# Optimization experiments

Measured on AMD Instinct MI355X. Metric: run time of the kernel, lower is better.

## Reference

```python
import jax, jax.numpy as jnp
import numpy as np

EPS = 1e-12
B, S, H, NH, L, F = 8, 512, 768, 12, 12, 3072
V, TV, P = 21128, 2, 512
DH = H // NH


def layer_norm(x, g, b):
    m = jnp.mean(x, axis=-1, keepdims=True)
    v = jnp.var(x, axis=-1, keepdims=True)
    return g * (x - m) / jnp.sqrt(v + EPS) + b


def setup_inputs() -> dict:
    key = jax.random.key(0)
    ks = iter(jax.random.split(key, 40))
    r = lambda shape: (jax.random.normal(next(ks), shape, jnp.float32) * 0.02)
    inp = {
        "input_ids": jax.random.randint(next(ks), (B, S), 0, V, jnp.int32),
        "segment_ids": jax.random.randint(next(ks), (B, S), 0, TV, jnp.int32),
        "attention_mask": jnp.ones((B, 1, 1, S), jnp.float32),
        "tok_emb": r((V, H)),
        "pos_emb": r((P, H)),
        "type_emb": r((TV, H)),
        "emb_g": jnp.ones((H,), jnp.float32),
        "emb_b": jnp.zeros((H,), jnp.float32),
        # stacked per-layer params [L, ...]
        "Wq": r((L, H, H)), "bq": jnp.zeros((L, H), jnp.float32),
        "Wk": r((L, H, H)), "bk": jnp.zeros((L, H), jnp.float32),
        "Wv": r((L, H, H)), "bv": jnp.zeros((L, H), jnp.float32),
        "Wao": r((L, H, H)), "bao": jnp.zeros((L, H), jnp.float32),
        "ln1_g": jnp.ones((L, H), jnp.float32), "ln1_b": jnp.zeros((L, H), jnp.float32),
        "Wi": r((L, H, F)), "bi": jnp.zeros((L, F), jnp.float32),
        "Wio": r((L, F, H)), "bio": jnp.zeros((L, H), jnp.float32),
        "ln2_g": jnp.ones((L, H), jnp.float32), "ln2_b": jnp.zeros((L, H), jnp.float32),
    }
    return inp


def reference(input_ids, segment_ids, attention_mask,
              tok_emb, pos_emb, type_emb, emb_g, emb_b,
              Wq, bq, Wk, bk, Wv, bv, Wao, bao, ln1_g, ln1_b,
              Wi, bi, Wio, bio, ln2_g, ln2_b):
    # ---- embedding: token + type + position, then LayerNorm ----
    x = tok_emb[input_ids] + type_emb[segment_ids] + pos_emb[None, :S, :]
    x = layer_norm(x, emb_g, emb_b)  # [B,S,H]

    mask_add = (1.0 - attention_mask) * -10000.0  # [B,1,1,S]
    scale = 1.0 / jnp.sqrt(jnp.asarray(DH, x.dtype))

    def split_heads(t):  # [B,S,H] -> [B,NH,S,DH]
        return t.reshape(B, S, NH, DH).transpose(0, 2, 1, 3)

    for l in range(Wq.shape[0]):
        q = split_heads(x @ Wq[l] + bq[l])
        k = split_heads(x @ Wk[l] + bk[l])
        v = split_heads(x @ Wv[l] + bv[l])
        score = jnp.einsum("bhqd,bhkd->bhqk", q, k) * scale + mask_add
        attn = jax.nn.softmax(score, axis=-1)
        ctx = jnp.einsum("bhqk,bhkd->bhqd", attn, v)
        ctx = ctx.transpose(0, 2, 1, 3).reshape(B, S, H)
        # attention output: dense + residual + LN
        attn_out = layer_norm(ctx @ Wao[l] + bao[l] + x, ln1_g[l], ln1_b[l])
        # FFN: dense-gelu-dense + residual + LN (exact erf gelu as in tf.keras)
        h = jax.nn.gelu(attn_out @ Wi[l] + bi[l], approximate=False)
        x = layer_norm(h @ Wio[l] + bio[l] + attn_out, ln2_g[l], ln2_b[l])

    return x  # sequence output [B,S,H]
```

## Files before the change

### kernel.cpp

```cpp
#include <hip/hip_runtime.h>
#include <math.h>

static constexpr int Bc = 8;
static constexpr int Sc = 512;
static constexpr int Hc = 768;
static constexpr int NHc = 12;
static constexpr int Lc = 12;
static constexpr int Fc = 3072;
static constexpr int DHc = 64;
static constexpr int NTOK = Bc * Sc;
static constexpr int QKVN = 3 * Hc;

static constexpr size_t W_QKV_OFF = 0;
static constexpr size_t W_AO_OFF  = 1769472;
static constexpr size_t W_I_OFF   = 2359296;
static constexpr size_t W_IO_OFF  = 4718592;
static constexpr size_t LW        = 7077888;

typedef _Float16 h16x8 __attribute__((ext_vector_type(8)));
typedef float f32x4 __attribute__((ext_vector_type(4)));
typedef unsigned short us4 __attribute__((ext_vector_type(4)));
typedef unsigned short us8 __attribute__((ext_vector_type(8)));
typedef unsigned int u32x4 __attribute__((ext_vector_type(4)));

__device__ __forceinline__ unsigned short f2h(float f) {
    _Float16 h = (_Float16)f;
    return __builtin_bit_cast(unsigned short, h);
}
__device__ __forceinline__ float h2f(unsigned short u) {
    return (float)__builtin_bit_cast(_Float16, u);
}

#define AS1 __attribute__((address_space(1)))
#define AS3 __attribute__((address_space(3)))
__device__ __forceinline__ void gld_lds16(const void* g, void* l) {
    __builtin_amdgcn_global_load_lds((const AS1 void*)g, (AS3 void*)l, 16, 0, 0);
}

__global__ __launch_bounds__(256) void prep_kernel(
    const float* __restrict__ Wq, const float* __restrict__ Wk,
    const float* __restrict__ Wv, const float* __restrict__ Wao,
    const float* __restrict__ Wi, const float* __restrict__ Wio,
    const float* __restrict__ bq, const float* __restrict__ bk,
    const float* __restrict__ bv, unsigned short* __restrict__ WALL,
    float* __restrict__ BALL)
{
    int t = blockIdx.x, l = blockIdx.y;
    int tid = threadIdx.x;

    if (t >= 432) {
        int idx = (t - 432) * 256 + tid;
        float v = (idx < 768) ? bq[l * Hc + idx]
                : (idx < 1536) ? bk[l * Hc + idx - 768]
                               : bv[l * Hc + idx - 1536];
        BALL[(size_t)l * QKVN + idx] = v;
        return;
    }

    const float* src;
    unsigned short* dst;
    int K, N, nkt, local;
    if (t < 144) {
        int mat = t / 36; local = t % 36;
        K = 768; N = 768; nkt = 3;
        src = (mat == 0 ? Wq : mat == 1 ? Wk : mat == 2 ? Wv : Wao) + (size_t)l * 589824;
        dst = WALL + (size_t)l * LW + (mat < 3 ? (size_t)mat * 589824 : W_AO_OFF);
    } else if (t < 288) {
        local = t - 144; K = 768; N = 3072; nkt = 3;
        src = Wi + (size_t)l * 2359296;
        dst = WALL + (size_t)l * LW + W_I_OFF;
    } else {
        local = t - 288; K = 3072; N = 768; nkt = 12;
        src = Wio + (size_t)l * 2359296;
        dst = WALL + (size_t)l * LW + W_IO_OFF;
    }
    int n0 = (local / nkt) * 64, k0 = (local % nkt) * 256;

    __shared__ float tl[64][65];
    int tx = tid & 15, ty = tid >> 4;
    int s_own = (tid >> 3) & 3;
    int c8    = tid & 7;
    int rb    = tid >> 5;

    us8 o[8];
    for (int s = 0; s < 4; s++) {
        int ks = k0 + s * 64;
#pragma unroll
        for (int j = 0; j < 4; j++) {
            int k = ty + j * 16;
            float4 v = *(const float4*)(src + (size_t)(ks + k) * N + n0 + tx * 4);
            tl[k][tx * 4 + 0] = v.x; tl[k][tx * 4 + 1] = v.y;
            tl[k][tx * 4 + 2] = v.z; tl[k][tx * 4 + 3] = v.w;
        }
        __syncthreads();
        if (s == s_own) {
#pragma unroll
            for (int it = 0; it < 8; it++) {
                int r = rb + it * 8;
#pragma unroll
                for (int j = 0; j < 8; j++) o[it][j] = f2h(tl[c8 * 8 + j][r]);
            }
        }
        __syncthreads();
    }
#pragma unroll
    for (int it = 0; it < 8; it++) {
        int r = rb + it * 8;
        *(us8*)(dst + (size_t)(n0 + r) * K + k0 + s_own * 64 + c8 * 8) = o[it];
    }
}

__device__ __forceinline__ void ln_stats192(float4 v, float& mean, float& rstd) {
    float s = v.x + v.y + v.z + v.w;
    float s2 = v.x * v.x + v.y * v.y + v.z * v.z + v.w * v.w;
#pragma unroll
    for (int o = 32; o > 0; o >>= 1) { s += __shfl_xor(s, o); s2 += __shfl_xor(s2, o); }
    __shared__ float red[6];
    int lane = threadIdx.x & 63, wid = threadIdx.x >> 6;
    if (lane == 0) { red[wid] = s; red[3 + wid] = s2; }
    __syncthreads();
    float ts  = red[0] + red[1] + red[2];
    float ts2 = red[3] + red[4] + red[5];
    mean = ts * (1.0f / Hc);
    float var = ts2 * (1.0f / Hc) - mean * mean;
    rstd = rsqrtf(var + 1e-12f);
}

__global__ __launch_bounds__(192) void embed_ln_kernel(
    const int* __restrict__ ids, const int* __restrict__ seg,
    const float* __restrict__ tok, const float* __restrict__ typ,
    const float* __restrict__ pos, const float* __restrict__ g,
    const float* __restrict__ b, float* __restrict__ outf,
    unsigned short* __restrict__ outb)
{
    int t = blockIdx.x;
    int si = t % Sc;
    int id = ids[t], sg = seg[t];
    int i = threadIdx.x;

    float4 tv = *(const float4*)(tok + (size_t)id * Hc + 4 * i);
    float4 yv = *(const float4*)(typ + (size_t)sg * Hc + 4 * i);
    float4 pv = *(const float4*)(pos + (size_t)si * Hc + 4 * i);
    float4 v = make_float4(tv.x + yv.x + pv.x, tv.y + yv.y + pv.y,
                           tv.z + yv.z + pv.z, tv.w + yv.w + pv.w);
    float mean, rstd;
    ln_stats192(v, mean, rstd);

    float4 gv = *(const float4*)(g + 4 * i);
    float4 bv = *(const float4*)(b + 4 * i);
    float4 o = make_float4(gv.x * (v.x - mean) * rstd + bv.x,
                           gv.y * (v.y - mean) * rstd + bv.y,
                           gv.z * (v.z - mean) * rstd + bv.z,
                           gv.w * (v.w - mean) * rstd + bv.w);
    *(float4*)(outf + (size_t)t * Hc + 4 * i) = o;
    us4 ob; ob[0] = f2h(o.x); ob[1] = f2h(o.y); ob[2] = f2h(o.z); ob[3] = f2h(o.w);
    *(us4*)(outb + (size_t)t * Hc + 4 * i) = ob;
}

__global__ __launch_bounds__(192) void add_ln2h_kernel(
    const unsigned short* __restrict__ t0, const unsigned short* __restrict__ t1,
    const float* __restrict__ res, const float* __restrict__ g,
    const float* __restrict__ b, float* __restrict__ outf,
    unsigned short* __restrict__ outb)
{
    int t = blockIdx.x;
    int i = threadIdx.x;
    us4 a = *(const us4*)(t0 + (size_t)t * Hc + 4 * i);
    us4 c = *(const us4*)(t1 + (size_t)t * Hc + 4 * i);
    float4 r = *(const float4*)(res + (size_t)t * Hc + 4 * i);
    float4 v = make_float4(h2f(a[0]) + h2f(c[0]) + r.x,
                           h2f(a[1]) + h2f(c[1]) + r.y,
                           h2f(a[2]) + h2f(c[2]) + r.z,
                           h2f(a[3]) + h2f(c[3]) + r.w);
    float mean, rstd;
    ln_stats192(v, mean, rstd);

    float4 gv = *(const float4*)(g + 4 * i);
    float4 bv = *(const float4*)(b + 4 * i);
    float4 o = make_float4(gv.x * (v.x - mean) * rstd + bv.x,
                           gv.y * (v.y - mean) * rstd + bv.y,
                           gv.z * (v.z - mean) * rstd + bv.z,
                           gv.w * (v.w - mean) * rstd + bv.w);
    *(float4*)(outf + (size_t)t * Hc + 4 * i) = o;
    us4 ob; ob[0] = f2h(o.x); ob[1] = f2h(o.y); ob[2] = f2h(o.z); ob[3] = f2h(o.w);
    *(us4*)(outb + (size_t)t * Hc + 4 * i) = ob;
}

template <int OUT>
__global__ __launch_bounds__(256) void gemm_mfma(
    const unsigned short* __restrict__ A,
    const unsigned short* __restrict__ Bt,
    const float* __restrict__ bias,
    unsigned short* __restrict__ Cb,
    unsigned short* __restrict__ VTp,
    int M, int N, int K, int kspan)
{
    __shared__ __align__(16) unsigned short As[128 * 64];
    __shared__ __align__(16) unsigned short Bs[128 * 64];

    int tid = threadIdx.x;
    int l = tid & 63, w = tid >> 6;

    int nbx = gridDim.x;
    int nwg = nbx * gridDim.y;
    int bid = blockIdx.y * nbx + blockIdx.x;
    if ((nwg & 7) == 0) {
        int cpx = nwg >> 3;
        bid = (bid & 7) * cpx + (bid >> 3);
    }
    int m0 = (bid % nbx) * 128, n0 = (bid / nbx) * 128;

    int lr = l & 15;
    int kg = l >> 4;
    int wr = (w >> 1) * 64, wc = (w & 1) * 64;
    int lx = lr & 7;
    int kbeg = blockIdx.z * kspan;

    f32x4 acc[4][4] = {};

    for (int k0 = kbeg; k0 < kbeg + kspan; k0 += 64) {
#pragma unroll
        for (int p = 0; p < 4; p++) {
            int i = p * 256 + w * 64 + l;
            int row = i >> 3;
            int slot = (i & 7) ^ (row & 7);
            const unsigned short* ga = A + (size_t)(m0 + row) * K + k0 + slot * 8;
            const unsigned short* gb = Bt + (size_t)(n0 + row) * K + k0 + slot * 8;
            unsigned short* la = As + (size_t)(p * 256 + w * 64) * 8;
            unsigned short* lb = Bs + (size_t)(p * 256 + w * 64) * 8;
            gld_lds16(ga, la);
            gld_lds16(gb, lb);
        }
        asm volatile("s_waitcnt vmcnt(0)" ::: "memory");
        __syncthreads();

#pragma unroll
        for (int kh = 0; kh < 2; kh++) {
            h16x8 av[4], bv[4];
#pragma unroll
            for (int f = 0; f < 4; f++) {
                int sl = (kh * 4 + kg) ^ lx;
                av[f] = *(const h16x8*)(As + (wr + f * 16 + lr) * 64 + sl * 8);
                bv[f] = *(const h16x8*)(Bs + (wc + f * 16 + lr) * 64 + sl * 8);
            }
#pragma unroll
            for (int i = 0; i < 4; i++)
#pragma unroll
                for (int j = 0; j < 4; j++)
                    acc[i][j] = __builtin_amdgcn_mfma_f32_16x16x32_f16(
                        av[i], bv[j], acc[i][j], 0, 0, 0);
        }
        __syncthreads();
    }

#pragma unroll
    for (int i = 0; i < 4; i++) {
        int rbase = m0 + wr + i * 16 + kg * 4;
#pragma unroll
        for (int j = 0; j < 4; j++) {
            int col = n0 + wc + j * 16 + lr;
            float bcol = (OUT == 4 && blockIdx.z > 0) ? 0.f : bias[col];
            if (OUT == 3 && col >= 1536) {
                int vcol = col - 1536;
                int hh = vcol >> 6, d = vcol & 63;
                int bbb = rbase >> 9, s0 = rbase & 511;
                us4 ob;
#pragma unroll
                for (int r = 0; r < 4; r++) ob[r] = f2h(acc[i][j][r] + bcol);
                *(us4*)(VTp + ((((size_t)bbb * NHc + hh) * DHc + d) << 9) + s0) = ob;
            } else if (OUT == 4) {
                unsigned short* op = Cb + (size_t)blockIdx.z * M * N;
#pragma unroll
                for (int r = 0; r < 4; r++)
                    op[(size_t)(rbase + r) * N + col] = f2h(acc[i][j][r] + bcol);
            } else {
                int ldc = (OUT == 3) ? 1536 : N;
#pragma unroll
                for (int r = 0; r < 4; r++) {
                    float v = acc[i][j][r] + bcol;
                    if (OUT == 1) v = 0.5f * v * (1.0f + erff(v * 0.70710678118654752f));
                    Cb[(size_t)(rbase + r) * ldc + col] = f2h(v);
                }
            }
        }
    }
}

__global__ __launch_bounds__(256) void attn_mfma(
    const unsigned short* __restrict__ QK, const unsigned short* __restrict__ VT,
    const float* __restrict__ mask, unsigned short* __restrict__ O)
{
    const int LD = 1536;
    __shared__ __align__(16) unsigned short Ks[64 * 64];
    __shared__ __align__(16) unsigned short Vt[64 * 64];
    __shared__ float Ml[64];

    int tid = threadIdx.x;
    int l = tid & 63, w = tid >> 6;
    int g = l >> 4, c = l & 15;
    int q0 = blockIdx.x * 64;
    int h = blockIdx.y, bb = blockIdx.z;

    const size_t rowQ = (size_t)(bb * Sc + q0 + w * 16 + c) * LD + h * DHc;
    h16x8 qv[2];
    qv[0] = *(const h16x8*)(QK + rowQ + 8 * g);
    qv[1] = *(const h16x8*)(QK + rowQ + 32 + 8 * g);

    float m_run = -1e30f, l_run = 0.f;
    f32x4 acc_o[4] = {};
    const float scale = 0.125f;

    for (int kt = 0; kt < Sc; kt += 64) {
        const unsigned short* Kgb = QK + (size_t)(bb * Sc + kt) * LD + Hc + h * DHc;
#pragma unroll
        for (int p = 0; p < 2; p++) {
            int i = p * 256 + tid;
            int row = i >> 3;
            int slot = (i & 7) ^ (row & 7);
            gld_lds16(Kgb + (size_t)row * LD + slot * 8, Ks + (size_t)(p * 256 + w * 64) * 8);
        }
        const unsigned short* Vg = VT + (((size_t)bb * NHc + h) * DHc << 9) + kt;
#pragma unroll
        for (int p = 0; p < 2; p++) {
            int i = p * 256 + tid;
            int row = i >> 3;
            int slot = (i & 7) ^ (row & 7);
            gld_lds16(Vg + ((size_t)row << 9) + slot * 8, Vt + (size_t)(p * 256 + w * 64) * 8);
        }
        if (tid < 64) Ml[tid] = (1.0f - mask[bb * Sc + kt + tid]) * -10000.0f;
        asm volatile("s_waitcnt vmcnt(0)" ::: "memory");
        __syncthreads();

        f32x4 s[4] = {};
#pragma unroll
        for (int kh = 0; kh < 2; kh++) {
#pragma unroll
            for (int f = 0; f < 4; f++) {
                int row = f * 16 + c;
                h16x8 av = *(const h16x8*)(Ks + row * 64 + (((kh * 4 + g) ^ (row & 7)) * 8));
                s[f] = __builtin_amdgcn_mfma_f32_16x16x32_f16(av, qv[kh], s[f], 0, 0, 0);
            }
        }

        f32x4 mv[4];
#pragma unroll
        for (int f = 0; f < 4; f++) mv[f] = *(const f32x4*)&Ml[f * 16 + 4 * g];
        float mx = -1e30f;
#pragma unroll
        for (int f = 0; f < 4; f++)
#pragma unroll
            for (int r = 0; r < 4; r++) {
                float sv = s[f][r] * scale + mv[f][r];
                s[f][r] = sv;
                mx = fmaxf(mx, sv);
            }
        mx = fmaxf(mx, __shfl_xor(mx, 16));
        mx = fmaxf(mx, __shfl_xor(mx, 32));
        float mn = fmaxf(m_run, mx);
        float fs = __expf(m_run - mn);
        m_run = mn;
        float ps = 0.f;
        f32x4 p[4];
#pragma unroll
        for (int f = 0; f < 4; f++)
#pragma unroll
            for (int r = 0; r < 4; r++) {
                float pv = __expf(s[f][r] - mn);
                p[f][r] = pv;
                ps += pv;
            }
        ps += __shfl_xor(ps, 16);
        ps += __shfl_xor(ps, 32);
        l_run = l_run * fs + ps;
#pragma unroll
        for (int fm = 0; fm < 4; fm++)
#pragma unroll
            for (int r = 0; r < 4; r++) acc_o[fm][r] *= fs;

        unsigned pk[4][2];
#pragma unroll
        for (int f = 0; f < 4; f++)
#pragma unroll
            for (int rp = 0; rp < 2; rp++)
                pk[f][rp] = ((unsigned)f2h(p[f][2 * rp + 1]) << 16) | f2h(p[f][2 * rp]);

#pragma unroll
        for (int kh = 0; kh < 2; kh++) {
            u32x4 bw;
#pragma unroll
            for (int t = 0; t < 4; t++) {
                int srcl = (2 * ((l >> 4) & 1) + (t >> 1)) * 16 + c;
                unsigned lo = __shfl(pk[2 * kh][t & 1], srcl);
                unsigned hi = __shfl(pk[2 * kh + 1][t & 1], srcl);
                bw[t] = (g & 2) ? hi : lo;
            }
            h16x8 bfrag = __builtin_bit_cast(h16x8, bw);
#pragma unroll
            for (int fm = 0; fm < 4; fm++) {
                int row = fm * 16 + c;
                h16x8 av = *(const h16x8*)(Vt + row * 64 + (((kh * 4 + g) ^ (row & 7)) * 8));
                acc_o[fm] = __builtin_amdgcn_mfma_f32_16x16x32_f16(av, bfrag, acc_o[fm], 0, 0, 0);
            }
        }
        __syncthreads();
    }

    float rl = 1.0f / l_run;
    size_t tokrow = (size_t)(bb * Sc + q0 + w * 16 + c) * Hc + h * DHc;
#pragma unroll
    for (int fm = 0; fm < 4; fm++) {
        us4 ob;
#pragma unroll
        for (int r = 0; r < 4; r++) ob[r] = f2h(acc_o[fm][r] * rl);
        *(us4*)(O + tokrow + fm * 16 + 4 * g) = ob;
    }
}

extern "C" void kernel_launch(void* const* d_in, const int* in_sizes, int n_in,
                              void* d_out, int out_size, void* d_ws, size_t ws_size,
                              hipStream_t stream)
{
    const int*   input_ids      = (const int*)  d_in[0];
    const int*   segment_ids    = (const int*)  d_in[1];
    const float* attention_mask = (const float*)d_in[2];
    const float* tok_emb = (const float*)d_in[3];
    const float* pos_emb = (const float*)d_in[4];
    const float* type_emb= (const float*)d_in[5];
    const float* emb_g   = (const float*)d_in[6];
    const float* emb_b   = (const float*)d_in[7];
    const float* Wq  = (const float*)d_in[8];  const float* bq  = (const float*)d_in[9];
    const float* Wk  = (const float*)d_in[10]; const float* bk  = (const float*)d_in[11];
    const float* Wv  = (const float*)d_in[12]; const float* bv  = (const float*)d_in[13];
    const float* Wao = (const float*)d_in[14]; const float* bao = (const float*)d_in[15];
    const float* ln1_g = (const float*)d_in[16]; const float* ln1_b = (const float*)d_in[17];
    const float* Wi  = (const float*)d_in[18]; const float* bi  = (const float*)d_in[19];
    const float* Wio = (const float*)d_in[20]; const float* bio = (const float*)d_in[21];
    const float* ln2_g = (const float*)d_in[22]; const float* ln2_b = (const float*)d_in[23];

    float* out = (float*)d_out;

    const size_t NT = (size_t)NTOK * Hc;
    float* Xf   = (float*)d_ws;
    float* XAf  = Xf + NT;
    float* BALL = XAf + NT;
    unsigned short* QKb = (unsigned short*)(BALL + (size_t)Lc * QKVN);
    unsigned short* VT  = QKb + (size_t)NTOK * 1536;
    unsigned short* Xb  = VT + NT;
    unsigned short* XAb = Xb + NT;
    unsigned short* Cb  = XAb + NT;
    unsigned short* Tp  = Cb + NT;
    unsigned short* Hb  = Tp + 2 * NT;
    unsigned short* WALL = Hb + (size_t)NTOK * Fc;

    prep_kernel<<<dim3(441, Lc), 256, 0, stream>>>(Wq, Wk, Wv, Wao, Wi, Wio,
                                                   bq, bk, bv, WALL, BALL);

    embed_ln_kernel<<<NTOK, 192, 0, stream>>>(input_ids, segment_ids, tok_emb,
                                              type_emb, pos_emb, emb_g, emb_b, Xf, Xb);

    dim3 gQKV(NTOK / 128, QKVN / 128);
    dim3 gF(NTOK / 128, Fc / 128);
    dim3 gH2(NTOK / 128, Hc / 128, 2);
    dim3 gA(Sc / 64, NHc, Bc);

    for (int l = 0; l < Lc; l++) {
        const unsigned short* WqkvT = WALL + (size_t)l * LW + W_QKV_OFF;
        const unsigned short* WaoT  = WALL + (size_t)l * LW + W_AO_OFF;
        const unsigned short* WiT   = WALL + (size_t)l * LW + W_I_OFF;
        const unsigned short* WioT  = WALL + (size_t)l * LW + W_IO_OFF;
        const float* bqkv = BALL + (size_t)l * QKVN;

        gemm_mfma<3><<<gQKV, 256, 0, stream>>>(Xb, WqkvT, bqkv, QKb, VT,
                                               NTOK, QKVN, Hc, Hc);
        attn_mfma<<<gA, 256, 0, stream>>>(QKb, VT, attention_mask, Cb);

        gemm_mfma<4><<<gH2, 256, 0, stream>>>(Cb, WaoT, bao + (size_t)l * Hc, Tp,
                                              nullptr, NTOK, Hc, Hc, Hc / 2);
        add_ln2h_kernel<<<NTOK, 192, 0, stream>>>(Tp, Tp + NT, Xf,
                                                  ln1_g + (size_t)l * Hc,
                                                  ln1_b + (size_t)l * Hc, XAf, XAb);

        gemm_mfma<1><<<gF, 256, 0, stream>>>(XAb, WiT, bi + (size_t)l * Fc, Hb,
                                             nullptr, NTOK, Fc, Hc, Hc);
        gemm_mfma<4><<<gH2, 256, 0, stream>>>(Hb, WioT, bio + (size_t)l * Hc, Tp,
                                              nullptr, NTOK, Hc, Fc, Fc / 2);
        float* xout = (l == Lc - 1) ? out : Xf;
        add_ln2h_kernel<<<NTOK, 192, 0, stream>>>(Tp, Tp + NT, XAf,
                                                  ln2_g + (size_t)l * Hc,
                                                  ln2_b + (size_t)l * Hc, xout, Xb);
    }
}
```

Before: 2.041 ms.

## Finer-grained weight prep, polynomial GELU, 128-key attention tiles with lazy rescale

The weight-conversion kernel now launches four times as many blocks, each transposing one 64x64 tile instead of looping over four, to get more parallelism. The exact erff in the FFN GELU epilogue is replaced by the Abramowitz-Stegun polynomial approximation using a hardware reciprocal and exp. This costs some accuracy, about 1e-7 in erf. Attention now processes 128 keys per iteration, doubling LDS tiles, and skips the online-softmax rescale unless the running max grows by more than 8, which cuts exp and multiply work.

```diff
diff --git a/kernel.cpp b/kernel.cpp
--- a/kernel.cpp
+++ b/kernel.cpp
@@ -31,6 +31,17 @@
     return (float)__builtin_bit_cast(_Float16, u);
 }
 
+__device__ __forceinline__ float gelu_fast(float v) {
+    float z = v * 0.70710678118654752f;
+    float az = fabsf(z);
+    float t = __builtin_amdgcn_rcpf(fmaf(0.3275911f, az, 1.0f));
+    float poly = fmaf(fmaf(fmaf(fmaf(1.061405429f, t, -1.453152027f), t,
+                    1.421413741f), t, -0.284496736f), t, 0.254829592f) * t;
+    float erf = 1.0f - poly * __expf(-az * az);
+    erf = (z < 0.f) ? -erf : erf;
+    return 0.5f * v * (1.0f + erf);
+}
+
 #define AS1 __attribute__((address_space(1)))
 #define AS3 __attribute__((address_space(3)))
 __device__ __forceinline__ void gld_lds16(const void* g, void* l) {
@@ -48,8 +59,8 @@
     int t = blockIdx.x, l = blockIdx.y;
     int tid = threadIdx.x;
 
-    if (t >= 432) {
-        int idx = (t - 432) * 256 + tid;
+    if (t >= 1728) {
+        int idx = (t - 1728) * 256 + tid;
         float v = (idx < 768) ? bq[l * Hc + idx]
                 : (idx < 1536) ? bk[l * Hc + idx - 768]
                                : bv[l * Hc + idx - 1536];
@@ -59,54 +70,41 @@
 
     const float* src;
     unsigned short* dst;
-    int K, N, nkt, local;
-    if (t < 144) {
-        int mat = t / 36; local = t % 36;
-        K = 768; N = 768; nkt = 3;
+    int K, N, ntn, local;
+    if (t < 576) {
+        int mat = t / 144; local = t % 144;
+        K = 768; N = 768; ntn = 12;
         src = (mat == 0 ? Wq : mat == 1 ? Wk : mat == 2 ? Wv : Wao) + (size_t)l * 589824;
         dst = WALL + (size_t)l * LW + (mat < 3 ? (size_t)mat * 589824 : W_AO_OFF);
-    } else if (t < 288) {
-        local = t - 144; K = 768; N = 3072; nkt = 3;
+    } else if (t < 1152) {
+        local = t - 576; K = 768; N = 3072; ntn = 48;
         src = Wi + (size_t)l * 2359296;
         dst = WALL + (size_t)l * LW + W_I_OFF;
     } else {
-        local = t - 288; K = 3072; N = 768; nkt = 12;
+        local = t - 1152; K = 3072; N = 768; ntn = 12;
         src = Wio + (size_t)l * 2359296;
         dst = WALL + (size_t)l * LW + W_IO_OFF;
     }
-    int n0 = (local / nkt) * 64, k0 = (local % nkt) * 256;
+    int n0 = (local % ntn) * 64, k0 = (local / ntn) * 64;
 
     __shared__ float tl[64][65];
     int tx = tid & 15, ty = tid >> 4;
-    int s_own = (tid >> 3) & 3;
-    int c8    = tid & 7;
-    int rb    = tid >> 5;
-
-    us8 o[8];
-    for (int s = 0; s < 4; s++) {
-        int ks = k0 + s * 64;
-#pragma unroll
-        for (int j = 0; j < 4; j++) {
-            int k = ty + j * 16;
-            float4 v = *(const float4*)(src + (size_t)(ks + k) * N + n0 + tx * 4);
-            tl[k][tx * 4 + 0] = v.x; tl[k][tx * 4 + 1] = v.y;
-            tl[k][tx * 4 + 2] = v.z; tl[k][tx * 4 + 3] = v.w;
-        }
-        __syncthreads();
-        if (s == s_own) {
-#pragma unroll
-            for (int it = 0; it < 8; it++) {
-                int r = rb + it * 8;
-#pragma unroll
-                for (int j = 0; j < 8; j++) o[it][j] = f2h(tl[c8 * 8 + j][r]);
-            }
-        }
-        __syncthreads();
-    }
-#pragma unroll
-    for (int it = 0; it < 8; it++) {
-        int r = rb + it * 8;
-        *(us8*)(dst + (size_t)(n0 + r) * K + k0 + s_own * 64 + c8 * 8) = o[it];
+#pragma unroll
+    for (int j = 0; j < 4; j++) {
+        int k = ty + j * 16;
+        float4 v = *(const float4*)(src + (size_t)(k0 + k) * N + n0 + tx * 4);
+        tl[k][tx * 4 + 0] = v.x; tl[k][tx * 4 + 1] = v.y;
+        tl[k][tx * 4 + 2] = v.z; tl[k][tx * 4 + 3] = v.w;
+    }
+    __syncthreads();
+#pragma unroll
+    for (int q = 0; q < 2; q++) {
+        int chunk = q * 256 + tid;
+        int row = chunk >> 3, c = chunk & 7;
+        us8 o;
+#pragma unroll
+        for (int j = 0; j < 8; j++) o[j] = f2h(tl[c * 8 + j][row]);
+        *(us8*)(dst + (size_t)(n0 + row) * K + k0 + c * 8) = o;
     }
 }
 
@@ -278,7 +276,7 @@
 #pragma unroll
                 for (int r = 0; r < 4; r++) {
                     float v = acc[i][j][r] + bcol;
-                    if (OUT == 1) v = 0.5f * v * (1.0f + erff(v * 0.70710678118654752f));
+                    if (OUT == 1) v = gelu_fast(v);
                     Cb[(size_t)(rbase + r) * ldc + col] = f2h(v);
                 }
             }
@@ -291,9 +289,9 @@
     const float* __restrict__ mask, unsigned short* __restrict__ O)
 {
     const int LD = 1536;
-    __shared__ __align__(16) unsigned short Ks[64 * 64];
-    __shared__ __align__(16) unsigned short Vt[64 * 64];
-    __shared__ float Ml[64];
+    __shared__ __align__(16) unsigned short Ks[128 * 64];
+    __shared__ __align__(16) unsigned short Vt[64 * 128];
+    __shared__ float Ml[128];
 
     int tid = threadIdx.x;
     int l = tid & 63, w = tid >> 6;
@@ -310,10 +308,10 @@
     f32x4 acc_o[4] = {};
     const float scale = 0.125f;
 
-    for (int kt = 0; kt < Sc; kt += 64) {
+    for (int kt = 0; kt < Sc; kt += 128) {
         const unsigned short* Kgb = QK + (size_t)(bb * Sc + kt) * LD + Hc + h * DHc;
 #pragma unroll
-        for (int p = 0; p < 2; p++) {
+        for (int p = 0; p < 4; p++) {
             int i = p * 256 + tid;
             int row = i >> 3;
             int slot = (i & 7) ^ (row & 7);
@@ -321,84 +319,85 @@
         }
         const unsigned short* Vg = VT + (((size_t)bb * NHc + h) * DHc << 9) + kt;
 #pragma unroll
-        for (int p = 0; p < 2; p++) {
+        for (int p = 0; p < 4; p++) {
             int i = p * 256 + tid;
-            int row = i >> 3;
-            int slot = (i & 7) ^ (row & 7);
+            int row = i >> 4;
+            int slot = (i & 15) ^ (row & 15);
             gld_lds16(Vg + ((size_t)row << 9) + slot * 8, Vt + (size_t)(p * 256 + w * 64) * 8);
         }
-        if (tid < 64) Ml[tid] = (1.0f - mask[bb * Sc + kt + tid]) * -10000.0f;
+        if (tid < 128) Ml[tid] = (1.0f - mask[bb * Sc + kt + tid]) * -10000.0f;
         asm volatile("s_waitcnt vmcnt(0)" ::: "memory");
         __syncthreads();
 
-        f32x4 s[4] = {};
+        f32x4 s[8] = {};
 #pragma unroll
         for (int kh = 0; kh < 2; kh++) {
 #pragma unroll
-            for (int f = 0; f < 4; f++) {
+            for (int f = 0; f < 8; f++) {
                 int row = f * 16 + c;
                 h16x8 av = *(const h16x8*)(Ks + row * 64 + (((kh * 4 + g) ^ (row & 7)) * 8));
                 s[f] = __builtin_amdgcn_mfma_f32_16x16x32_f16(av, qv[kh], s[f], 0, 0, 0);
             }
         }
 
-        f32x4 mv[4];
-#pragma unroll
-        for (int f = 0; f < 4; f++) mv[f] = *(const f32x4*)&Ml[f * 16 + 4 * g];
         float mx = -1e30f;
 #pragma unroll
-        for (int f = 0; f < 4; f++)
+        for (int f = 0; f < 8; f++) {
+            f32x4 mv = *(const f32x4*)&Ml[f * 16 + 4 * g];
 #pragma unroll
             for (int r = 0; r < 4; r++) {
-                float sv = s[f][r] * scale + mv[f][r];
+                float sv = s[f][r] * scale + mv[r];
                 s[f][r] = sv;
                 mx = fmaxf(mx, sv);
             }
+        }
         mx = fmaxf(mx, __shfl_xor(mx, 16));
         mx = fmaxf(mx, __shfl_xor(mx, 32));
-        float mn = fmaxf(m_run, mx);
-        float fs = __expf(m_run - mn);
-        m_run = mn;
+        if (!__all(mx - m_run <= 8.0f)) {
+            float mn = fmaxf(m_run, mx);
+            float fs = __expf(m_run - mn);
+            m_run = mn;
+            l_run *= fs;
+#pragma unroll
+            for (int fm = 0; fm < 4; fm++)
+#pragma unroll
+                for (int r = 0; r < 4; r++) acc_o[fm][r] *= fs;
+        }
         float ps = 0.f;
-        f32x4 p[4];
-#pragma unroll
-        for (int f = 0; f < 4; f++)
+#pragma unroll
+        for (int f = 0; f < 8; f++)
 #pragma unroll
             for (int r = 0; r < 4; r++) {
-                float pv = __expf(s[f][r] - mn);
-                p[f][r] = pv;
+                float pv = __expf(s[f][r] - m_run);
+                s[f][r] = pv;
                 ps += pv;
             }
         ps += __shfl_xor(ps, 16);
         ps += __shfl_xor(ps, 32);
-        l_run = l_run * fs + ps;
-#pragma unroll
-        for (int fm = 0; fm < 4; fm++)
-#pragma unroll
-            for (int r = 0; r < 4; r++) acc_o[fm][r] *= fs;
-
-        unsigned pk[4][2];
-#pragma unroll
-        for (int f = 0; f < 4; f++)
+        l_run += ps;
+
+        unsigned pk[8][2];
+#pragma unroll
+        for (int f = 0; f < 8; f++)
 #pragma unroll
             for (int rp = 0; rp < 2; rp++)
-                pk[f][rp] = ((unsigned)f2h(p[f][2 * rp + 1]) << 16) | f2h(p[f][2 * rp]);
-
-#pragma unroll
-        for (int kh = 0; kh < 2; kh++) {
+                pk[f][rp] = ((unsigned)f2h(s[f][2 * rp + 1]) << 16) | f2h(s[f][2 * rp]);
+
+#pragma unroll
+        for (int kh2 = 0; kh2 < 4; kh2++) {
             u32x4 bw;
 #pragma unroll
             for (int t = 0; t < 4; t++) {
                 int srcl = (2 * ((l >> 4) & 1) + (t >> 1)) * 16 + c;
-                unsigned lo = __shfl(pk[2 * kh][t & 1], srcl);
-                unsigned hi = __shfl(pk[2 * kh + 1][t & 1], srcl);
+                unsigned lo = __shfl(pk[2 * kh2][t & 1], srcl);
+                unsigned hi = __shfl(pk[2 * kh2 + 1][t & 1], srcl);
                 bw[t] = (g & 2) ? hi : lo;
             }
             h16x8 bfrag = __builtin_bit_cast(h16x8, bw);
 #pragma unroll
             for (int fm = 0; fm < 4; fm++) {
                 int row = fm * 16 + c;
-                h16x8 av = *(const h16x8*)(Vt + row * 64 + (((kh * 4 + g) ^ (row & 7)) * 8));
+                h16x8 av = *(const h16x8*)(Vt + row * 128 + (((kh2 * 4 + g) ^ (row & 15)) * 8));
                 acc_o[fm] = __builtin_amdgcn_mfma_f32_16x16x32_f16(av, bfrag, acc_o[fm], 0, 0, 0);
             }
         }
@@ -452,8 +451,8 @@
     unsigned short* Hb  = Tp + 2 * NT;
     unsigned short* WALL = Hb + (size_t)NTOK * Fc;
 
-    prep_kernel<<<dim3(441, Lc), 256, 0, stream>>>(Wq, Wk, Wv, Wao, Wi, Wio,
-                                                   bq, bk, bv, WALL, BALL);
+    prep_kernel<<<dim3(1737, Lc), 256, 0, stream>>>(Wq, Wk, Wv, Wao, Wi, Wio,
+                                                    bq, bk, bv, WALL, BALL);
 
     embed_ln_kernel<<<NTOK, 192, 0, stream>>>(input_ids, segment_ids, tok_emb,
                                               type_emb, pos_emb, emb_g, emb_b, Xf, Xb);
```

Result: slower. 2.194 ms (+7.5%).
